# Kernel tuning notes

Measured on AMD Instinct MI355X. Metric: run time of the kernel, lower is better.

Reference implementation:

```python
import jax, jax.numpy as jnp
import numpy as np

N = 100000   # nodes
F = 256      # input features
H = 64       # hidden dims
C = 40       # classes
L = 4        # GGNN layers
E = 1200000  # edges


def setup_inputs() -> dict:
    key = jax.random.key(0)
    ks = jax.random.split(key, 8)
    x = jax.random.normal(ks[0], (N, F), dtype=jnp.float32)
    edge_index = jax.random.randint(ks[1], (2, E), 0, N, dtype=jnp.int64)
    # glorot-initialized projection weights
    weight_in = jax.random.uniform(ks[2], (F, H), jnp.float32, -1.0, 1.0) * np.sqrt(6.0 / (F + H))
    weight_out = jax.random.uniform(ks[3], (H, C), jnp.float32, -1.0, 1.0) * np.sqrt(6.0 / (H + C))
    # GatedGraphConv: per-layer message weight [L, H, H], shared GRUCell params
    conv_weight = jax.random.uniform(ks[4], (L, H, H), jnp.float32, -1.0, 1.0) * np.sqrt(6.0 / (2 * H))
    s = 1.0 / np.sqrt(H)
    w_ih = jax.random.uniform(ks[5], (3 * H, H), jnp.float32, -s, s)
    w_hh = jax.random.uniform(ks[6], (3 * H, H), jnp.float32, -s, s)
    b_ih = jax.random.uniform(ks[7], (3 * H,), jnp.float32, -s, s)
    b_hh = jnp.zeros((3 * H,), jnp.float32)
    return {"x": x, "edge_index": edge_index, "weight_in": weight_in,
            "weight_out": weight_out, "conv_weight": conv_weight,
            "w_ih": w_ih, "w_hh": w_hh, "b_ih": b_ih, "b_hh": b_hh}


def _gru_cell(a, h, w_ih, w_hh, b_ih, b_hh):
    # torch.nn.GRUCell math: input a, hidden h
    gi = a @ w_ih.T + b_ih
    gh = h @ w_hh.T + b_hh
    i_r, i_z, i_n = jnp.split(gi, 3, axis=1)
    h_r, h_z, h_n = jnp.split(gh, 3, axis=1)
    r = jax.nn.sigmoid(i_r + h_r)
    z = jax.nn.sigmoid(i_z + h_z)
    n = jnp.tanh(i_n + r * h_n)
    return (1.0 - z) * n + z * h


def reference(x, edge_index, weight_in, weight_out, conv_weight, w_ih, w_hh, b_ih, b_hh):
    n_nodes = x.shape[0]
    src, dst = edge_index[0], edge_index[1]
    h = x @ weight_in  # [N, H]
    for i in range(conv_weight.shape[0]):
        m = h @ conv_weight[i]                                   # [N, H]
        agg = jax.ops.segment_sum(m[src], dst, num_segments=n_nodes)  # scatter-add
        h = _gru_cell(agg, h, w_ih, w_hh, b_ih, b_hh)
    out = h @ weight_out  # [N, C]
    return jax.nn.log_softmax(out, axis=1)
```

## Files before the change

kernel.cpp:

```cpp
#include <hip/hip_runtime.h>


#define DEVI __device__ __forceinline__

typedef __attribute__((ext_vector_type(8))) short short8;
typedef __attribute__((ext_vector_type(4))) float f32x4;

constexpr int N_NODES   = 100000;
constexpr int F_IN      = 256;
constexpr int H_DIM     = 64;
constexpr int C_OUT     = 40;
constexpr int ROW_TILES = N_NODES / 16;
constexpr int CH        = 8192;
constexpr int NBUCK     = (N_NODES + 127) / 128;
constexpr int LB_STRIDE = NBUCK + 1;
constexpr int BCAP      = 2048;

DEVI float bf2f(unsigned short u) {
    unsigned v = ((unsigned)u) << 16;
    float f; __builtin_memcpy(&f, &v, 4); return f;
}
DEVI unsigned short f2bf(float f) {
    unsigned u; __builtin_memcpy(&u, &f, 4);
    unsigned r = u + 0x7FFFu + ((u >> 16) & 1u);
    return (unsigned short)(r >> 16);
}
DEVI float in_elem(const void* p, size_t idx, int f32flag) {
    return f32flag ? ((const float*)p)[idx]
                   : bf2f(((const unsigned short*)p)[idx]);
}
DEVI short8 f32row_to_frag(const float* __restrict__ p) {
    const f32x4* q = (const f32x4*)p;
    f32x4 lo = q[0], hi = q[1];
    short8 a;
    a[0] = (short)f2bf(lo[0]); a[1] = (short)f2bf(lo[1]);
    a[2] = (short)f2bf(lo[2]); a[3] = (short)f2bf(lo[3]);
    a[4] = (short)f2bf(hi[0]); a[5] = (short)f2bf(hi[1]);
    a[6] = (short)f2bf(hi[2]); a[7] = (short)f2bf(hi[3]);
    return a;
}

__global__ void detect_kernel(const void* x, const int* ei, int* flags) {
    if (threadIdx.x != 0 || blockIdx.x != 0) return;
    const unsigned short* u = (const unsigned short*)x;
    int sane = 0;
    for (int i = 0; i < 256; ++i) {
        int e = (u[i] >> 7) & 0xFF;
        if (e >= 100 && e <= 145) sane++;
    }
    flags[0] = (sane < 230) ? 1 : 0;
    int zeros = 0;
    for (int i = 0; i < 64; ++i)
        if (ei[2 * i + 1] == 0) zeros++;
    flags[1] = (zeros >= 63) ? 1 : 0;
}

__global__ __launch_bounds__(256) void bucket_local(
        const int* __restrict__ ei, int E, const int* __restrict__ flags,
        int* __restrict__ wgsorted,
        int* __restrict__ lbase_g) {
    __shared__ int hist[NBUCK];
    __shared__ int partial[256];
    __shared__ int staging[CH];
    int tid = threadIdx.x, wg = blockIdx.x;
    int i64 = flags[1];
    int base = wg * CH;
    int cnt_wg = min(CH, E - base);

    for (int i = tid; i < NBUCK; i += 256) hist[i] = 0;
    __syncthreads();
    for (int k = tid; k < cnt_wg; k += 256) {
        size_t e = (size_t)base + k;
        int d = i64 ? ei[2 * ((size_t)E + e)] : ei[(size_t)E + e];
        atomicAdd(&hist[d >> 7], 1);
    }
    __syncthreads();
    int i0 = 4 * tid;
    int e0 = (i0 + 0 < NBUCK) ? hist[i0 + 0] : 0;
    int e1 = (i0 + 1 < NBUCK) ? hist[i0 + 1] : 0;
    int e2 = (i0 + 2 < NBUCK) ? hist[i0 + 2] : 0;
    int e3 = (i0 + 3 < NBUCK) ? hist[i0 + 3] : 0;
    int s0 = e0, s1 = s0 + e1, s2 = s1 + e2, s3 = s2 + e3;
    __syncthreads();
    partial[tid] = s3;
    __syncthreads();
    for (int ofs = 1; ofs < 256; ofs <<= 1) {
        int add = (tid >= ofs) ? partial[tid - ofs] : 0;
        __syncthreads();
        partial[tid] += add;
        __syncthreads();
    }
    int pbase = (tid > 0) ? partial[tid - 1] : 0;
    if (i0 + 0 < NBUCK) hist[i0 + 0] = pbase;
    if (i0 + 1 < NBUCK) hist[i0 + 1] = pbase + s0;
    if (i0 + 2 < NBUCK) hist[i0 + 2] = pbase + s1;
    if (i0 + 3 < NBUCK) hist[i0 + 3] = pbase + s2;
    __syncthreads();
    int* lb = lbase_g + (size_t)wg * LB_STRIDE;
    for (int i = tid; i < NBUCK; i += 256) lb[i] = hist[i];
    if (tid == 0) lb[NBUCK] = cnt_wg;
    __syncthreads();
    for (int k = tid; k < cnt_wg; k += 256) {
        size_t e = (size_t)base + k;
        int s, d;
        if (i64) { s = ei[2 * e]; d = ei[2 * ((size_t)E + e)]; }
        else     { s = ei[e];     d = ei[(size_t)E + e]; }
        int pos = atomicAdd(&hist[d >> 7], 1);
        staging[pos] = ((d & 127) << 17) | s;
    }
    __syncthreads();
    for (int k = tid; k < cnt_wg; k += 256)
        wgsorted[(size_t)base + k] = staging[k];
}

__global__ __launch_bounds__(256) void bucket_csr(
        const int* __restrict__ wgsorted,
        const int* __restrict__ lbase_g,
        int nwg,
        int* __restrict__ rowptr,
        int* __restrict__ counts,
        int* __restrict__ esrc) {
    __shared__ int segofs[256];
    __shared__ int edata[BCAP];
    __shared__ int sout[BCAP];
    __shared__ int hist2[128];
    __shared__ int cur2[128];
    int tid = threadIdx.x, b = blockIdx.x;

    int lbv = 0, cntv = 0;
    if (tid < nwg) {
        const int* lb = lbase_g + (size_t)tid * LB_STRIDE;
        lbv  = lb[b];
        cntv = lb[b + 1] - lbv;
    }
    segofs[tid] = cntv;
    __syncthreads();
    for (int ofs = 1; ofs < 256; ofs <<= 1) {
        int add = (tid >= ofs) ? segofs[tid - ofs] : 0;
        __syncthreads();
        segofs[tid] += add;
        __syncthreads();
    }
    int tot = segofs[255];
    int myofs = (tid > 0) ? segofs[tid - 1] : 0;
    if (tot > BCAP) tot = BCAP;
    if (tid < nwg && cntv > 0) {
        const int* srcp = wgsorted + (size_t)tid * CH + lbv;
        for (int i = 0; i < cntv; ++i) {
            int o = myofs + i;
            if (o < BCAP) edata[o] = srcp[i];
        }
    }
    if (tid < 128) hist2[tid] = 0;
    __syncthreads();
    for (int i = tid; i < tot; i += 256) atomicAdd(&hist2[edata[i] >> 17], 1);
    __syncthreads();
    if (tid < 128) cur2[tid] = hist2[tid];
    __syncthreads();
    for (int ofs = 1; ofs < 128; ofs <<= 1) {
        int add = 0;
        if (tid < 128 && tid >= ofs) add = cur2[tid - ofs];
        __syncthreads();
        if (tid < 128) cur2[tid] += add;
        __syncthreads();
    }
    int nodeexcl = 0;
    if (tid < 128) nodeexcl = (tid > 0) ? cur2[tid - 1] : 0;
    __syncthreads();
    if (tid < 128) {
        int node = b * 128 + tid;
        if (node < N_NODES) {
            counts[node] = hist2[tid];
            rowptr[node] = b * BCAP + nodeexcl;
        }
        cur2[tid] = nodeexcl;
    }
    __syncthreads();
    for (int i = tid; i < tot; i += 256) {
        int p = edata[i];
        int pos = atomicAdd(&cur2[p >> 17], 1);
        sout[pos] = p & 0x1FFFF;
    }
    __syncthreads();
    for (int i = tid; i < tot; i += 256)
        esrc[(size_t)b * BCAP + i] = sout[i];
}

__global__ void prep_bfrag(const void* __restrict__ src,
                           unsigned short* __restrict__ dst,
                           int K, int npad_tiles, int ncols_real,
                           const int* __restrict__ flags) {
    int f32 = flags[0];
    int t = blockIdx.x * blockDim.x + threadIdx.x;
    int total = (K / 32) * npad_tiles * 512;
    if (t >= total) return;
    int i    = t & 7;
    int lane = (t >> 3) & 63;
    int jt   = (t >> 9) % npad_tiles;
    int kb   = t / (512 * npad_tiles);
    int k    = kb * 32 + ((lane >> 4) << 3) + i;
    int col  = jt * 16 + (lane & 15);
    unsigned short v = 0;
    if (col < ncols_real) v = f2bf(in_elem(src, (size_t)k * ncols_real + col, f32));
    dst[t] = v;
}

__global__ __launch_bounds__(64) void wcomb_kernel(
        const void* __restrict__ conv_w, const void* __restrict__ w_ih,
        unsigned short* __restrict__ wcomb, const int* __restrict__ flags) {
    int f32 = flags[0];
    int lane = threadIdx.x;
    int c = blockIdx.x;
    int l = blockIdx.y;
    int kb = c / 12, jt = c % 12;
    int quad = lane >> 4, l15 = lane & 15;
    int g = jt * 16 + l15;
    unsigned short* dst = wcomb + (size_t)l * 12288 + ((size_t)c * 64 + lane) * 8;
#pragma unroll
    for (int i = 0; i < 8; ++i) {
        int k = kb * 32 + quad * 8 + i;
        float acc = 0.0f;
        for (int j = 0; j < 64; ++j)
            acc += in_elem(conv_w, (size_t)l * 4096 + k * 64 + j, f32) *
                   in_elem(w_ih, (size_t)g * 64 + j, f32);
        dst[i] = f2bf(acc);
    }
}

__global__ void prep_gruw(const void* __restrict__ w_hh,
                          const void* __restrict__ b_ih,
                          const void* __restrict__ b_hh,
                          unsigned short* __restrict__ whh_c,
                          unsigned short* __restrict__ bias_c,
                          const int* __restrict__ flags) {
    int f32 = flags[0];
    int t = blockIdx.x * blockDim.x + threadIdx.x;
    if (t < 12288)            whh_c[t]          = f2bf(in_elem(w_hh, t, f32));
    else if (t < 12288 + 192) bias_c[t - 12288] = f2bf(in_elem(b_ih, t - 12288, f32));
    else if (t < 12288 + 384) bias_c[t - 12288] = f2bf(in_elem(b_hh, t - 12480, f32));
}

template <int XF32>
DEVI void proj_in_body(const void* __restrict__ xr,
                       const unsigned short* __restrict__ wfrag,
                       unsigned short* __restrict__ h) {
    int wid = blockIdx.x * 4 + (threadIdx.x >> 6);
    if (wid >= ROW_TILES) return;
    int lane = threadIdx.x & 63;
    int l15 = lane & 15, quad = lane >> 4;
    int row0 = wid * 16;
    int arow = row0 + l15;

    f32x4 acc[4];
#pragma unroll
    for (int jt = 0; jt < 4; ++jt) acc[jt] = (f32x4)(0.0f);

#pragma unroll
    for (int kb = 0; kb < 8; ++kb) {
        short8 a;
        if (XF32)
            a = f32row_to_frag((const float*)xr + (size_t)arow * F_IN + kb * 32 + quad * 8);
        else
            a = *(const short8*)((const unsigned short*)xr + (size_t)arow * F_IN + kb * 32 + quad * 8);
#pragma unroll
        for (int jt = 0; jt < 4; ++jt) {
            short8 b = *(const short8*)(wfrag + (size_t)((kb * 4 + jt) * 64 + lane) * 8);
            acc[jt] = __builtin_amdgcn_mfma_f32_16x16x32_bf16(a, b, acc[jt], 0, 0, 0);
        }
    }
#pragma unroll
    for (int jt = 0; jt < 4; ++jt)
#pragma unroll
        for (int r = 0; r < 4; ++r)
            h[(size_t)(row0 + quad * 4 + r) * H_DIM + jt * 16 + l15] = f2bf(acc[jt][r]);
}

__global__ __launch_bounds__(256) void proj_in_kernel(
        const void* __restrict__ x,
        const unsigned short* __restrict__ wfrag,
        unsigned short* __restrict__ h,
        const int* __restrict__ flags) {
    if (flags[0]) proj_in_body<1>(x, wfrag, h);
    else          proj_in_body<0>(x, wfrag, h);
}

__global__ __launch_bounds__(256) void gather_agg(
        const unsigned short* __restrict__ h,
        const int* __restrict__ rowptr,
        const int* __restrict__ counts,
        const int* __restrict__ esrc,
        unsigned short* __restrict__ aggB) {
    int n = blockIdx.x * 4 + (threadIdx.x >> 6);
    if (n >= N_NODES) return;
    int j = threadIdx.x & 63;
    int start = rowptr[n];
    int deg   = counts[n];
    float a0 = 0.f, a1 = 0.f, a2 = 0.f, a3 = 0.f;
    int i = 0;
    for (; i + 4 <= deg; i += 4) {
        int s0 = esrc[start + i],     s1 = esrc[start + i + 1];
        int s2 = esrc[start + i + 2], s3 = esrc[start + i + 3];
        a0 += bf2f(h[(size_t)s0 * H_DIM + j]);
        a1 += bf2f(h[(size_t)s1 * H_DIM + j]);
        a2 += bf2f(h[(size_t)s2 * H_DIM + j]);
        a3 += bf2f(h[(size_t)s3 * H_DIM + j]);
    }
    for (; i < deg; ++i)
        a0 += bf2f(h[(size_t)esrc[start + i] * H_DIM + j]);
    aggB[(size_t)n * H_DIM + j] = f2bf((a0 + a1) + (a2 + a3));
}

__global__ __launch_bounds__(256) void gru_kernel(
        const unsigned short* __restrict__ aggB,
        unsigned short* __restrict__ h,
        const unsigned short* __restrict__ wcomb_l,
        const unsigned short* __restrict__ whh_c,
        const unsigned short* __restrict__ bias_c) {
    int wid = blockIdx.x * 4 + (threadIdx.x >> 6);
    if (wid >= ROW_TILES) return;
    int lane = threadIdx.x & 63;
    int l15 = lane & 15, quad = lane >> 4;
    int row0 = wid * 16;
    int arow = row0 + l15;

    f32x4 gi[12], gh[12];
#pragma unroll
    for (int jt = 0; jt < 12; ++jt) { gi[jt] = (f32x4)(0.0f); gh[jt] = (f32x4)(0.0f); }

#pragma unroll
    for (int kb = 0; kb < 2; ++kb) {
        short8 aa = *(const short8*)(aggB + (size_t)arow * H_DIM + kb * 32 + quad * 8);
        short8 ah = *(const short8*)(h + (size_t)arow * H_DIM + kb * 32 + quad * 8);
#pragma unroll
        for (int jt = 0; jt < 12; ++jt) {
            short8 bi = *(const short8*)(wcomb_l + (size_t)((kb * 12 + jt) * 64 + lane) * 8);
            gi[jt] = __builtin_amdgcn_mfma_f32_16x16x32_bf16(aa, bi, gi[jt], 0, 0, 0);
            short8 bh = *(const short8*)(whh_c + (size_t)(jt * 16 + l15) * H_DIM + kb * 32 + quad * 8);
            gh[jt] = __builtin_amdgcn_mfma_f32_16x16x32_bf16(ah, bh, gh[jt], 0, 0, 0);
        }
    }

#pragma unroll
    for (int jc = 0; jc < 4; ++jc) {
        int j = jc * 16 + l15;
        float bir = bf2f(bias_c[j]),       bhr = bf2f(bias_c[192 + j]);
        float biz = bf2f(bias_c[64 + j]),  bhz = bf2f(bias_c[256 + j]);
        float bin = bf2f(bias_c[128 + j]), bhn = bf2f(bias_c[320 + j]);
#pragma unroll
        for (int r = 0; r < 4; ++r) {
            int row = row0 + quad * 4 + r;
            float xr = (gi[jc][r] + bir) + (gh[jc][r] + bhr);
            float xz = (gi[4 + jc][r] + biz) + (gh[4 + jc][r] + bhz);
            float in_ = gi[8 + jc][r] + bin;
            float hn_ = gh[8 + jc][r] + bhn;
            xr = fminf(fmaxf(xr, -30.0f), 30.0f);
            xz = fminf(fmaxf(xz, -30.0f), 30.0f);
            float rg = 1.0f / (1.0f + __expf(-xr));
            float zg = 1.0f / (1.0f + __expf(-xz));
            float na = in_ + rg * hn_;
            float ey = __expf(-2.0f * fabsf(na));
            float th = (1.0f - ey) / (1.0f + ey);
            float nt = (na < 0.0f) ? -th : th;
            float ho = bf2f(h[(size_t)row * H_DIM + j]);
            h[(size_t)row * H_DIM + j] = f2bf((1.0f - zg) * nt + zg * ho);
        }
    }
}

__global__ __launch_bounds__(256) void projout_kernel(
        const unsigned short* __restrict__ h,
        const unsigned short* __restrict__ wofrag,
        void* __restrict__ out,
        const int* __restrict__ flags) {
    int f32out = flags[0];
    int wid = blockIdx.x * 4 + (threadIdx.x >> 6);
    if (wid >= ROW_TILES) return;
    int lane = threadIdx.x & 63;
    int l15 = lane & 15, quad = lane >> 4;
    int row0 = wid * 16;
    int arow = row0 + l15;

    f32x4 acc[3];
#pragma unroll
    for (int jt = 0; jt < 3; ++jt) acc[jt] = (f32x4)(0.0f);

#pragma unroll
    for (int kb = 0; kb < 2; ++kb) {
        short8 a = *(const short8*)(h + (size_t)arow * H_DIM + kb * 32 + quad * 8);
#pragma unroll
        for (int jt = 0; jt < 3; ++jt) {
            short8 b = *(const short8*)(wofrag + (size_t)((kb * 3 + jt) * 64 + lane) * 8);
            acc[jt] = __builtin_amdgcn_mfma_f32_16x16x32_bf16(a, b, acc[jt], 0, 0, 0);
        }
    }

    float* of = (float*)out;
    unsigned short* ob = (unsigned short*)out;
    bool valid2 = (l15 < 8);
#pragma unroll
    for (int r = 0; r < 4; ++r) {
        int row = row0 + quad * 4 + r;
        float v0 = acc[0][r], v1 = acc[1][r], v2 = acc[2][r];
        float mx = fmaxf(v0, v1);
        if (valid2) mx = fmaxf(mx, v2);
#pragma unroll
        for (int d = 1; d < 16; d <<= 1) mx = fmaxf(mx, __shfl_xor(mx, d));
        float s = __expf(v0 - mx) + __expf(v1 - mx) + (valid2 ? __expf(v2 - mx) : 0.0f);
#pragma unroll
        for (int d = 1; d < 16; d <<= 1) s += __shfl_xor(s, d);
        float lg = mx + __logf(s);
        size_t o0 = (size_t)row * C_OUT + l15;
        if (f32out) {
            of[o0]      = v0 - lg;
            of[o0 + 16] = v1 - lg;
            if (valid2) of[o0 + 32] = v2 - lg;
        } else {
            ob[o0]      = f2bf(v0 - lg);
            ob[o0 + 16] = f2bf(v1 - lg);
            if (valid2) ob[o0 + 32] = f2bf(v2 - lg);
        }
    }
}

extern "C" void kernel_launch(void* const* d_in, const int* in_sizes, int n_in,
                              void* d_out, int out_size, void* d_ws, size_t ws_size,
                              hipStream_t stream) {
    const void* x      = d_in[0];
    const int*  ei     = (const int*)d_in[1];
    const void* w_in   = d_in[2];
    const void* w_out  = d_in[3];
    const void* conv_w = d_in[4];
    const void* w_ih   = d_in[5];
    const void* w_hh   = d_in[6];
    const void* b_ih   = d_in[7];
    const void* b_hh   = d_in[8];

    const int E   = in_sizes[1] / 2;
    const int nwg = (E + CH - 1) / CH;

    char* ws = (char*)d_ws;
    size_t off = 0;
    auto carve = [&](size_t bytes) {
        void* p = ws + off;
        off += (bytes + 255) & ~(size_t)255;
        return p;
    };
    int*            flags    = (int*)carve(256);
    unsigned short* aggB     = (unsigned short*)carve((size_t)N_NODES * H_DIM * 2);
    unsigned short* hbuf     = (unsigned short*)carve((size_t)N_NODES * H_DIM * 2);
    int*            counts   = (int*)carve((size_t)N_NODES * 4);
    int*            rowptr   = (int*)carve((size_t)N_NODES * 4);
    int*            wgsorted = (int*)carve((size_t)nwg * CH * 4);
    int*            lbase_g  = (int*)carve((size_t)nwg * LB_STRIDE * 4);
    int*            esrcP    = (int*)carve((size_t)NBUCK * BCAP * 4);
    unsigned short* winfrag  = (unsigned short*)carve((size_t)8 * 4 * 512 * 2);
    unsigned short* wcomb    = (unsigned short*)carve((size_t)4 * 12288 * 2);
    unsigned short* wofrag   = (unsigned short*)carve((size_t)3072 * 2);
    unsigned short* whh_c    = (unsigned short*)carve((size_t)12288 * 2);
    unsigned short* bias_c   = (unsigned short*)carve((size_t)384 * 2);

    detect_kernel<<<1, 64, 0, stream>>>(x, ei, flags);

    bucket_local<<<nwg, 256, 0, stream>>>(ei, E, flags, wgsorted, lbase_g);
    bucket_csr<<<NBUCK, 256, 0, stream>>>(wgsorted, lbase_g, nwg,
                                          rowptr, counts, esrcP);

    prep_bfrag<<<64, 256, 0, stream>>>(w_in, winfrag, 256, 4, 64, flags);
    prep_bfrag<<<12, 256, 0, stream>>>(w_out, wofrag, 64, 3, 40, flags);
    wcomb_kernel<<<dim3(24, 4), 64, 0, stream>>>(conv_w, w_ih, wcomb, flags);
    prep_gruw<<<50, 256, 0, stream>>>(w_hh, b_ih, b_hh, whh_c, bias_c, flags);

    const int gblocks = (ROW_TILES + 3) / 4;
    const int nblocks = N_NODES / 4;

    proj_in_kernel<<<gblocks, 256, 0, stream>>>(x, winfrag, hbuf, flags);

    for (int l = 0; l < 4; ++l) {
        gather_agg<<<nblocks, 256, 0, stream>>>(hbuf, rowptr, counts, esrcP, aggB);
        gru_kernel<<<gblocks, 256, 0, stream>>>(aggB, hbuf, wcomb + (size_t)l * 12288,
                                                whh_c, bias_c);
    }

    projout_kernel<<<gblocks, 256, 0, stream>>>(hbuf, wofrag, d_out, flags);
}
```

Baseline: 638.4 us.

## Parallelize bucket gather, merge weight-prep kernels, unroll edge gather by eight

In bucket_csr, the segment gather used to run serially per work-group thread. It now copies edges in parallel across all threads, using a binary search over the inclusive prefix sum to find each edge's source segment. The four small weight-preparation launches are merged into one prep_all kernel to cut launch overhead. The neighbor gather loop in gather_agg gains an 8-way unrolled path with eight accumulators, giving more independent loads in flight at the cost of extra registers.

```diff
diff --git a/kernel.cpp b/kernel.cpp
--- a/kernel.cpp
+++ b/kernel.cpp
@@ -120,7 +120,8 @@
         int* __restrict__ rowptr,
         int* __restrict__ counts,
         int* __restrict__ esrc) {
-    __shared__ int segofs[256];
+    __shared__ int segincl[256];
+    __shared__ int segbase[256];
     __shared__ int edata[BCAP];
     __shared__ int sout[BCAP];
     __shared__ int hist2[128];
@@ -133,23 +134,24 @@
         lbv  = lb[b];
         cntv = lb[b + 1] - lbv;
     }
-    segofs[tid] = cntv;
+    segbase[tid] = lbv;
+    segincl[tid] = cntv;
     __syncthreads();
     for (int ofs = 1; ofs < 256; ofs <<= 1) {
-        int add = (tid >= ofs) ? segofs[tid - ofs] : 0;
+        int add = (tid >= ofs) ? segincl[tid - ofs] : 0;
         __syncthreads();
-        segofs[tid] += add;
+        segincl[tid] += add;
         __syncthreads();
     }
-    int tot = segofs[255];
-    int myofs = (tid > 0) ? segofs[tid - 1] : 0;
-    if (tot > BCAP) tot = BCAP;
-    if (tid < nwg && cntv > 0) {
-        const int* srcp = wgsorted + (size_t)tid * CH + lbv;
-        for (int i = 0; i < cntv; ++i) {
-            int o = myofs + i;
-            if (o < BCAP) edata[o] = srcp[i];
-        }
+    int tot = min(segincl[255], BCAP);
+    for (int i = tid; i < tot; i += 256) {
+        int lo = 0, hi = 255;
+        while (lo < hi) {
+            int mid = (lo + hi) >> 1;
+            if (segincl[mid] > i) hi = mid; else lo = mid + 1;
+        }
+        int excl = (lo > 0) ? segincl[lo - 1] : 0;
+        edata[i] = wgsorted[(size_t)lo * CH + segbase[lo] + (i - excl)];
     }
     if (tid < 128) hist2[tid] = 0;
     __syncthreads();
@@ -186,58 +188,62 @@
         esrc[(size_t)b * BCAP + i] = sout[i];
 }
 
-__global__ void prep_bfrag(const void* __restrict__ src,
-                           unsigned short* __restrict__ dst,
-                           int K, int npad_tiles, int ncols_real,
-                           const int* __restrict__ flags) {
+__global__ void prep_all(const void* __restrict__ w_in,
+                         const void* __restrict__ w_out,
+                         const void* __restrict__ w_hh,
+                         const void* __restrict__ b_ih,
+                         const void* __restrict__ b_hh,
+                         const void* __restrict__ conv_w,
+                         const void* __restrict__ w_ih,
+                         unsigned short* __restrict__ winfrag,
+                         unsigned short* __restrict__ wofrag,
+                         unsigned short* __restrict__ whh_c,
+                         unsigned short* __restrict__ bias_c,
+                         unsigned short* __restrict__ wcomb,
+                         const int* __restrict__ flags) {
     int f32 = flags[0];
     int t = blockIdx.x * blockDim.x + threadIdx.x;
-    int total = (K / 32) * npad_tiles * 512;
-    if (t >= total) return;
-    int i    = t & 7;
-    int lane = (t >> 3) & 63;
-    int jt   = (t >> 9) % npad_tiles;
-    int kb   = t / (512 * npad_tiles);
-    int k    = kb * 32 + ((lane >> 4) << 3) + i;
-    int col  = jt * 16 + (lane & 15);
-    unsigned short v = 0;
-    if (col < ncols_real) v = f2bf(in_elem(src, (size_t)k * ncols_real + col, f32));
-    dst[t] = v;
-}
-
-__global__ __launch_bounds__(64) void wcomb_kernel(
-        const void* __restrict__ conv_w, const void* __restrict__ w_ih,
-        unsigned short* __restrict__ wcomb, const int* __restrict__ flags) {
-    int f32 = flags[0];
-    int lane = threadIdx.x;
-    int c = blockIdx.x;
-    int l = blockIdx.y;
-    int kb = c / 12, jt = c % 12;
-    int quad = lane >> 4, l15 = lane & 15;
-    int g = jt * 16 + l15;
-    unsigned short* dst = wcomb + (size_t)l * 12288 + ((size_t)c * 64 + lane) * 8;
-#pragma unroll
-    for (int i = 0; i < 8; ++i) {
-        int k = kb * 32 + quad * 8 + i;
-        float acc = 0.0f;
-        for (int j = 0; j < 64; ++j)
-            acc += in_elem(conv_w, (size_t)l * 4096 + k * 64 + j, f32) *
-                   in_elem(w_ih, (size_t)g * 64 + j, f32);
-        dst[i] = f2bf(acc);
-    }
-}
-
-__global__ void prep_gruw(const void* __restrict__ w_hh,
-                          const void* __restrict__ b_ih,
-                          const void* __restrict__ b_hh,
-                          unsigned short* __restrict__ whh_c,
-                          unsigned short* __restrict__ bias_c,
-                          const int* __restrict__ flags) {
-    int f32 = flags[0];
-    int t = blockIdx.x * blockDim.x + threadIdx.x;
-    if (t < 12288)            whh_c[t]          = f2bf(in_elem(w_hh, t, f32));
-    else if (t < 12288 + 192) bias_c[t - 12288] = f2bf(in_elem(b_ih, t - 12288, f32));
-    else if (t < 12288 + 384) bias_c[t - 12288] = f2bf(in_elem(b_hh, t - 12480, f32));
+    if (t < 16384) {
+        int i = t & 7, lane = (t >> 3) & 63, jt = (t >> 9) & 3, kb = t >> 11;
+        int k = kb * 32 + ((lane >> 4) << 3) + i;
+        int col = jt * 16 + (lane & 15);
+        winfrag[t] = f2bf(in_elem(w_in, (size_t)k * 64 + col, f32));
+    } else if (t < 19456) {
+        int u = t - 16384;
+        int i = u & 7, lane = (u >> 3) & 63;
+        int jt = (u >> 9) % 3, kb = u / 1536;
+        int k = kb * 32 + ((lane >> 4) << 3) + i;
+        int col = jt * 16 + (lane & 15);
+        wofrag[u] = (col < 40) ? f2bf(in_elem(w_out, (size_t)k * 40 + col, f32))
+                               : (unsigned short)0;
+    } else if (t < 31744) {
+        int u = t - 19456;
+        whh_c[u] = f2bf(in_elem(w_hh, u, f32));
+    } else if (t < 31936) {
+        int u = t - 31744;
+        bias_c[u] = f2bf(in_elem(b_ih, u, f32));
+    } else if (t < 32128) {
+        int u = t - 31936;
+        bias_c[192 + u] = f2bf(in_elem(b_hh, u, f32));
+    } else if (t < 32128 + 6144) {
+        int u = t - 32128;
+        int lane = u & 63;
+        int c = (u >> 6) % 24;
+        int l = u / 1536;
+        int kb = c / 12, jt = c % 12;
+        int quad = lane >> 4, l15 = lane & 15;
+        int g = jt * 16 + l15;
+        unsigned short* dst = wcomb + (size_t)l * 12288 + ((size_t)c * 64 + lane) * 8;
+#pragma unroll
+        for (int i = 0; i < 8; ++i) {
+            int k = kb * 32 + quad * 8 + i;
+            float acc = 0.0f;
+            for (int j = 0; j < 64; ++j)
+                acc += in_elem(conv_w, (size_t)l * 4096 + k * 64 + j, f32) *
+                       in_elem(w_ih, (size_t)g * 64 + j, f32);
+            dst[i] = f2bf(acc);
+        }
+    }
 }
 
 template <int XF32>
@@ -296,7 +302,22 @@
     int start = rowptr[n];
     int deg   = counts[n];
     float a0 = 0.f, a1 = 0.f, a2 = 0.f, a3 = 0.f;
+    float a4 = 0.f, a5 = 0.f, a6 = 0.f, a7 = 0.f;
     int i = 0;
+    for (; i + 8 <= deg; i += 8) {
+        int s0 = esrc[start + i],     s1 = esrc[start + i + 1];
+        int s2 = esrc[start + i + 2], s3 = esrc[start + i + 3];
+        int s4 = esrc[start + i + 4], s5 = esrc[start + i + 5];
+        int s6 = esrc[start + i + 6], s7 = esrc[start + i + 7];
+        a0 += bf2f(h[(size_t)s0 * H_DIM + j]);
+        a1 += bf2f(h[(size_t)s1 * H_DIM + j]);
+        a2 += bf2f(h[(size_t)s2 * H_DIM + j]);
+        a3 += bf2f(h[(size_t)s3 * H_DIM + j]);
+        a4 += bf2f(h[(size_t)s4 * H_DIM + j]);
+        a5 += bf2f(h[(size_t)s5 * H_DIM + j]);
+        a6 += bf2f(h[(size_t)s6 * H_DIM + j]);
+        a7 += bf2f(h[(size_t)s7 * H_DIM + j]);
+    }
     for (; i + 4 <= deg; i += 4) {
         int s0 = esrc[start + i],     s1 = esrc[start + i + 1];
         int s2 = esrc[start + i + 2], s3 = esrc[start + i + 3];
@@ -307,7 +328,7 @@
     }
     for (; i < deg; ++i)
         a0 += bf2f(h[(size_t)esrc[start + i] * H_DIM + j]);
-    aggB[(size_t)n * H_DIM + j] = f2bf((a0 + a1) + (a2 + a3));
+    aggB[(size_t)n * H_DIM + j] = f2bf(((a0 + a1) + (a2 + a3)) + ((a4 + a5) + (a6 + a7)));
 }
 
 __global__ __launch_bounds__(256) void gru_kernel(
@@ -453,7 +474,7 @@
     int*            wgsorted = (int*)carve((size_t)nwg * CH * 4);
     int*            lbase_g  = (int*)carve((size_t)nwg * LB_STRIDE * 4);
     int*            esrcP    = (int*)carve((size_t)NBUCK * BCAP * 4);
-    unsigned short* winfrag  = (unsigned short*)carve((size_t)8 * 4 * 512 * 2);
+    unsigned short* winfrag  = (unsigned short*)carve((size_t)16384 * 2);
     unsigned short* wcomb    = (unsigned short*)carve((size_t)4 * 12288 * 2);
     unsigned short* wofrag   = (unsigned short*)carve((size_t)3072 * 2);
     unsigned short* whh_c    = (unsigned short*)carve((size_t)12288 * 2);
@@ -465,10 +486,9 @@
     bucket_csr<<<NBUCK, 256, 0, stream>>>(wgsorted, lbase_g, nwg,
                                           rowptr, counts, esrcP);
 
-    prep_bfrag<<<64, 256, 0, stream>>>(w_in, winfrag, 256, 4, 64, flags);
-    prep_bfrag<<<12, 256, 0, stream>>>(w_out, wofrag, 64, 3, 40, flags);
-    wcomb_kernel<<<dim3(24, 4), 64, 0, stream>>>(conv_w, w_ih, wcomb, flags);
-    prep_gruw<<<50, 256, 0, stream>>>(w_hh, b_ih, b_hh, whh_c, bias_c, flags);
+    prep_all<<<(32128 + 6144 + 255) / 256, 256, 0, stream>>>(
+        w_in, w_out, w_hh, b_ih, b_hh, conv_w, w_ih,
+        winfrag, wofrag, whh_c, bias_c, wcomb, flags);
 
     const int gblocks = (ROW_TILES + 3) / 4;
     const int nblocks = N_NODES / 4;
```

After: 627.4 us. No clear change (-1.7%).
